# Optimization experiments

Measured on AMD Instinct MI355X. Metric: run time of the kernel, lower is better.

## Reference

```python
import jax, jax.numpy as jnp
import numpy as np

NUM_GROUPS = 32
NUM_HEADS = 8  # channels=512 / num_head_channels=64
EPS = 1e-5


def group_norm(x, gamma, beta):
    # x: [B, C, T]
    b, c, t = x.shape
    xg = x.reshape(b, NUM_GROUPS, (c // NUM_GROUPS) * t)
    mean = xg.mean(axis=-1, keepdims=True)
    var = xg.var(axis=-1, keepdims=True)
    xg = (xg - mean) * jax.lax.rsqrt(var + EPS)
    return xg.reshape(b, c, t) * gamma[None, :, None] + beta[None, :, None]


def setup_inputs() -> dict:
    key = jax.random.key(0)
    ks = jax.random.split(key, 8)
    B, C, H, W = 16, 512, 32, 32
    E = 1024
    x = jax.random.normal(ks[0], (B, C, H, W), dtype=jnp.float32)
    emb = jax.random.normal(ks[1], (B, E), dtype=jnp.float32)
    gn_gamma = jnp.ones((C,), jnp.float32)
    gn_beta = jnp.zeros((C,), jnp.float32)
    # FiLM: Linear(emb_channels, 2*channels), weight init std=0.001, bias zero
    emb_w = jax.random.normal(ks[2], (2 * C, E), dtype=jnp.float32) * 0.001
    emb_b = jnp.zeros((2 * C,), jnp.float32)
    # conv1x1 qkv: [3C, C]
    qkv_w = jax.random.normal(ks[3], (3 * C, C), dtype=jnp.float32) * (1.0 / np.sqrt(C))
    qkv_b = jnp.zeros((3 * C,), jnp.float32)
    # proj_out conv1x1 (zero-init in original; use small random so grads flow)
    proj_w = jax.random.normal(ks[4], (C, C), dtype=jnp.float32) * 0.02
    proj_b = jnp.zeros((C,), jnp.float32)
    return dict(x=x, emb=emb, gn_gamma=gn_gamma, gn_beta=gn_beta,
                emb_w=emb_w, emb_b=emb_b, qkv_w=qkv_w, qkv_b=qkv_b,
                proj_w=proj_w, proj_b=proj_b)


def reference(x, emb, gn_gamma, gn_beta, emb_w, emb_b, qkv_w, qkv_b, proj_w, proj_b):
    b, c, h_sp, w_sp = x.shape
    t = h_sp * w_sp
    xr = x.reshape(b, c, t)
    h = group_norm(xr, gn_gamma, gn_beta)
    # FiLM conditioning
    e = jax.nn.silu(emb) @ emb_w.T + emb_b  # [B, 2C]
    scale, shift = jnp.split(e, 2, axis=1)
    h = h * (1.0 + scale[:, :, None]) + shift[:, :, None]
    # conv1x1 QKV
    qkv = jnp.einsum('oc,bct->bot', qkv_w, h) + qkv_b[None, :, None]  # [B, 3C, T]
    ch = c // NUM_HEADS
    qkv = qkv.reshape(b * NUM_HEADS, 3 * ch, t)  # legacy head ordering
    q, k, v = jnp.split(qkv, 3, axis=1)
    s = 1.0 / jnp.sqrt(jnp.sqrt(jnp.float32(ch)))
    w = jnp.einsum('bct,bcs->bts', q * s, k * s)  # [B*H, T, T]
    w = jax.nn.softmax(w, axis=-1)
    a = jnp.einsum('bts,bcs->bct', w, v).reshape(b, c, t)
    out = jnp.einsum('oc,bct->bot', proj_w, a) + proj_b[None, :, None]
    return (xr + out).reshape(b, c, h_sp, w_sp)
```

## Files before the change

kernel.cpp:

```cpp
#include <hip/hip_runtime.h>
#include <hip/hip_bf16.h>

typedef __hip_bfloat16 bf16;
typedef __attribute__((ext_vector_type(8))) short short8;
typedef __attribute__((ext_vector_type(4))) float f32x4;
typedef __attribute__((ext_vector_type(4))) unsigned short us4;
typedef __attribute__((ext_vector_type(2))) unsigned short us2;

#define B_  16
#define C_  512
#define T_  1024
#define G_  32
#define CPG 16
#define E_  1024
#define NH  8
#define CH  64
#define CT  (C_ * T_)

__device__ __forceinline__ float b2f(bf16 v) { return __bfloat162float(v); }
__device__ __forceinline__ unsigned short fbits_fast(float v) {
  unsigned int u = __builtin_bit_cast(unsigned int, v);
  u += 0x7fff + ((u >> 16) & 1);
  return (unsigned short)(u >> 16);
}
__device__ __forceinline__ bf16 f2b_fast(float v) {
  unsigned short s = fbits_fast(v);
  return *reinterpret_cast<bf16*>(&s);
}
__device__ __forceinline__ unsigned int cvtpk(float lo, float hi) {
  unsigned int r;
  asm("v_cvt_pk_bf16_f32 %0, %1, %2" : "=v"(r) : "v"(lo), "v"(hi));
  return r;
}

__device__ __forceinline__ void gload16(const void* g, void* l) {
  __builtin_amdgcn_global_load_lds(
      (const __attribute__((address_space(1))) void*)g,
      (__attribute__((address_space(3))) void*)l, 16, 0, 0);
}

__global__ __launch_bounds__(256) void convert_w_kernel(
    const float* __restrict__ qkv_w, const float* __restrict__ proj_w,
    bf16* __restrict__ wq, bf16* __restrict__ wp) {
  int i4 = blockIdx.x * 256 + threadIdx.x;
  const int NQ4 = (3 * C_ * C_) / 4;
  const float* src;
  unsigned short* dst;
  int off;
  if (i4 < NQ4) {
    src = qkv_w; dst = (unsigned short*)wq; off = i4;
  } else {
    src = proj_w; dst = (unsigned short*)wp; off = i4 - NQ4;
  }
  float4 v = *(const float4*)(src + (size_t)off * 4);
  uint2 pk = {cvtpk(v.x, v.y), cvtpk(v.z, v.w)};
  *(uint2*)(dst + (size_t)off * 4) = pk;
}

__global__ __launch_bounds__(256) void convert_one(
    const float* __restrict__ src, bf16* __restrict__ dst) {
  int i4 = blockIdx.x * 256 + threadIdx.x;
  float4 v = *(const float4*)(src + (size_t)i4 * 4);
  uint2 pk = {cvtpk(v.x, v.y), cvtpk(v.z, v.w)};
  *(uint2*)((unsigned short*)dst + (size_t)i4 * 4) = pk;
}

__global__ __launch_bounds__(256) void film2_kernel(
    const float* __restrict__ emb, const float* __restrict__ emb_w,
    const float* __restrict__ emb_b, float* __restrict__ e_out) {
  __shared__ float S[B_ * E_];
  int tid = threadIdx.x;
  float4* S4 = (float4*)S;
  const float4* e4 = (const float4*)emb;
  for (int i = tid; i < (B_ * E_) / 4; i += 256) {
    float4 v = e4[i];
    float4 o;
    o.x = v.x / (1.f + __expf(-v.x));
    o.y = v.y / (1.f + __expf(-v.y));
    o.z = v.z / (1.f + __expf(-v.z));
    o.w = v.w / (1.f + __expf(-v.w));
    S4[i] = o;
  }
  __syncthreads();
  int wave = tid >> 6, lane = tid & 63;
  int j = blockIdx.x * 4 + wave;
  const float4* w4p = (const float4*)(emb_w + (size_t)j * E_);
  float4 w4[4];
#pragma unroll
  for (int k = 0; k < 4; k++) w4[k] = w4p[k * 64 + lane];
  float bias = emb_b[j];
  for (int b = 0; b < B_; b++) {
    const float4* Sb = (const float4*)(S + b * E_);
    float acc = 0.f;
#pragma unroll
    for (int k = 0; k < 4; k++) {
      float4 s = Sb[k * 64 + lane];
      acc += w4[k].x * s.x + w4[k].y * s.y + w4[k].z * s.z + w4[k].w * s.w;
    }
#pragma unroll
    for (int off = 1; off < 64; off <<= 1) acc += __shfl_xor(acc, off, 64);
    if (lane == 0) e_out[b * (2 * C_) + j] = acc + bias;
  }
}

__global__ __launch_bounds__(1024) void gn_stats_kernel(
    const float* __restrict__ x, float* __restrict__ mean_buf,
    float* __restrict__ rstd_buf) {
  int bg = blockIdx.x;
  const float4* b4 = (const float4*)(x + (size_t)bg * (CPG * T_));
  int tid = threadIdx.x;
  float s = 0.f, sq = 0.f;
#pragma unroll
  for (int p = 0; p < 4; p++) {
    float4 v = b4[p * 1024 + tid];
    s += v.x + v.y + v.z + v.w;
    sq += v.x * v.x + v.y * v.y + v.z * v.z + v.w * v.w;
  }
  for (int off = 32; off > 0; off >>= 1) {
    s += __shfl_down(s, off, 64);
    sq += __shfl_down(sq, off, 64);
  }
  __shared__ float ss[16], ssq[16];
  int wid = tid >> 6, lane = tid & 63;
  if (lane == 0) { ss[wid] = s; ssq[wid] = sq; }
  __syncthreads();
  if (tid == 0) {
    float S = 0.f, Q = 0.f;
#pragma unroll
    for (int w = 0; w < 16; w++) { S += ss[w]; Q += ssq[w]; }
    const float inv_n = 1.f / (CPG * T_);
    float m = S * inv_n;
    float var = Q * inv_n - m * m;
    mean_buf[bg] = m;
    rstd_buf[bg] = rsqrtf(fmaxf(var, 0.f) + 1e-5f);
  }
}

__global__ __launch_bounds__(256) void norm_film_t2(
    const float* __restrict__ x, const float* __restrict__ mean_buf,
    const float* __restrict__ rstd_buf, const float* __restrict__ gamma,
    const float* __restrict__ beta, const float* __restrict__ e_buf,
    bf16* __restrict__ h, int b0) {
  __shared__ unsigned short S[64][66];
  __shared__ float pm[64], pr[64], pa[64];
  int t0 = blockIdx.x * 64;
  int c0 = blockIdx.y * 64;
  int bl = blockIdx.z;
  int b = b0 + bl;
  int tid = threadIdx.x;
  if (tid < 64) {
    int c = c0 + tid;
    int g = c >> 4;
    float m = mean_buf[b * G_ + g];
    float r = rstd_buf[b * G_ + g];
    float sc = 1.f + e_buf[b * 2 * C_ + c];
    float sh = e_buf[b * 2 * C_ + C_ + c];
    pm[tid] = m;
    pr[tid] = r * gamma[c] * sc;
    pa[tid] = beta[c] * sc + sh;
  }
  __syncthreads();
  const float* xb = x + ((size_t)b * C_ + c0) * T_ + t0;
#pragma unroll
  for (int p = 0; p < 4; p++) {
    int i = p * 256 + tid;
    int cl = i >> 4, t4 = (i & 15) * 4;
    float4 v = *(const float4*)(xb + (size_t)cl * T_ + t4);
    float m = pm[cl], r = pr[cl], ad = pa[cl];
    *(unsigned int*)&S[cl][t4] = cvtpk((v.x - m) * r + ad, (v.y - m) * r + ad);
    *(unsigned int*)&S[cl][t4 + 2] =
        cvtpk((v.z - m) * r + ad, (v.w - m) * r + ad);
  }
  __syncthreads();
  unsigned short* hg = (unsigned short*)h + ((size_t)bl * T_ + t0) * C_ + c0;
#pragma unroll
  for (int p = 0; p < 2; p++) {
    int i = p * 256 + tid;
    int tr = i >> 3, c8 = (i & 7) * 8;
    unsigned int w0 = (unsigned int)S[c8 + 0][tr] |
                      ((unsigned int)S[c8 + 1][tr] << 16);
    unsigned int w1 = (unsigned int)S[c8 + 2][tr] |
                      ((unsigned int)S[c8 + 3][tr] << 16);
    unsigned int w2 = (unsigned int)S[c8 + 4][tr] |
                      ((unsigned int)S[c8 + 5][tr] << 16);
    unsigned int w3 = (unsigned int)S[c8 + 6][tr] |
                      ((unsigned int)S[c8 + 7][tr] << 16);
    int4 pk = {(int)w0, (int)w1, (int)w2, (int)w3};
    *(int4*)(hg + (size_t)tr * C_ + c8) = pk;
  }
}

#define ST_STRIDE 264
__global__ __launch_bounds__(256) void qkv_gemm_mfma5(
    const bf16* __restrict__ h, const bf16* __restrict__ wq,
    const float* __restrict__ qkv_b, bf16* __restrict__ qb,
    bf16* __restrict__ kb, bf16* __restrict__ vb, int ngroups) {
  __shared__ __align__(16) unsigned short LB[40960];
  int bid = blockIdx.x;
  int g, o;
  if ((ngroups & 7) == 0) {
    int xcd = bid & 7, j = bid >> 3;
    o = j % 24;
    int slot = j / 24;
    g = slot * 8 + xcd;
  } else {
    o = bid % 24;
    g = bid / 24;
  }
  int tst = g & 3;
  int bl = g >> 2;
  int o0 = o * 64;
  int tb = tst * 256;
  int tid = threadIdx.x;
  int wave = tid >> 6, lane = tid & 63;
  int col = lane & 15, quad = lane >> 4;
  int cs = col & 7;
  int w64 = wave * 64;
  const unsigned short* hg = (const unsigned short*)h + (size_t)bl * T_ * C_;
  const unsigned short* wg = (const unsigned short*)wq;
  char* lds = (char*)LB;
  f32x4 acc[4][4];
  for (int i = 0; i < 4; i++)
    for (int j2 = 0; j2 < 4; j2++) acc[i][j2] = f32x4{0, 0, 0, 0};

#define QSTAGE(buf, c0_)                                                      \
  do {                                                                        \
    _Pragma("unroll") for (int p = 0; p < 8; p++) {                           \
      int i_ = p * 256 + tid;                                                 \
      int row_ = i_ >> 3;                                                     \
      int sci_ = (i_ & 7) ^ (row_ & 7);                                       \
      gload16(hg + (size_t)(tb + row_) * C_ + (c0_) + sci_ * 8,               \
              lds + (buf) * 40960 + (p * 256 + wave * 64) * 16);              \
    }                                                                         \
    _Pragma("unroll") for (int p = 0; p < 2; p++) {                           \
      int i_ = p * 256 + tid;                                                 \
      int row_ = i_ >> 3;                                                     \
      int sci_ = (i_ & 7) ^ (row_ & 7);                                       \
      gload16(wg + (size_t)(o0 + row_) * C_ + (c0_) + sci_ * 8,               \
              lds + (buf) * 40960 + 32768 + (p * 256 + wave * 64) * 16);      \
    }                                                                         \
  } while (0)

  QSTAGE(0, 0);
  __syncthreads();
  int cur = 0;
  for (int kst = 0; kst < 8; kst++) {
    if (kst < 7) QSTAGE(cur ^ 1, (kst + 1) * 64);
    const unsigned short* hb = LB + cur * 20480;
    const unsigned short* wb2 = hb + 16384;
    __builtin_amdgcn_s_setprio(1);
#pragma unroll
    for (int ks = 0; ks < 2; ks++) {
      short8 af[4], bfr[4];
#pragma unroll
      for (int mt = 0; mt < 4; mt++)
        af[mt] = *(const short8*)&hb[(w64 + mt * 16 + col) * 64 +
                                     (((ks * 4 + quad) ^ cs) << 3)];
#pragma unroll
      for (int nt = 0; nt < 4; nt++)
        bfr[nt] = *(const short8*)&wb2[(nt * 16 + col) * 64 +
                                       (((ks * 4 + quad) ^ cs) << 3)];
#pragma unroll
      for (int mt = 0; mt < 4; mt++)
#pragma unroll
        for (int nt = 0; nt < 4; nt++)
          acc[mt][nt] = __builtin_amdgcn_mfma_f32_16x16x32_bf16(
              af[mt], bfr[nt], acc[mt][nt], 0, 0, 0);
    }
    __builtin_amdgcn_s_setprio(0);
    __syncthreads();
    cur ^= 1;
  }
#undef QSTAGE
  int sec = (o0 >> 6) % 3;
  int hd = o0 / 192;
  const float s = 0.35355339059327373f;
  const float sq = s * 1.4426950408889634f;
  if (sec < 2) {
    bf16* dst = (sec == 0) ? qb : kb;
    float sc = (sec == 0) ? sq : s;
    size_t hb2 = (size_t)(bl * NH + hd) * T_ * CH;
    for (int mt = 0; mt < 4; mt++) {
      for (int r = 0; r < 4; r++) {
        int t = tb + w64 + mt * 16 + quad * 4 + r;
        for (int nt = 0; nt < 4; nt++) {
          int ch = nt * 16 + col;
          dst[hb2 + (size_t)t * CH + ch] =
              f2b_fast((acc[mt][nt][r] + qkv_b[o0 + ch]) * sc);
        }
      }
    }
  } else {
    for (int mt = 0; mt < 4; mt++) {
      for (int r = 0; r < 4; r++) {
        int tl = w64 + mt * 16 + quad * 4 + r;
        for (int nt = 0; nt < 4; nt++) {
          int ch = nt * 16 + col;
          LB[ch * ST_STRIDE + tl] =
              fbits_fast(acc[mt][nt][r] + qkv_b[o0 + ch]);
        }
      }
    }
    __syncthreads();
    int rr = tid >> 2, csx = (tid & 3) * 64;
    size_t base = ((size_t)(bl * NH + hd) * CH + rr) * T_ + tb + csx;
    unsigned short* vg = (unsigned short*)vb;
    for (int j2 = 0; j2 < 8; j2++)
      *(int4*)(vg + base + j2 * 8) =
          *(const int4*)&LB[rr * ST_STRIDE + csx + j2 * 8];
  }
}

__global__ __launch_bounds__(256, 4) void attn_mfma8(
    const bf16* __restrict__ qb, const bf16* __restrict__ kb,
    const bf16* __restrict__ vb, bf16* __restrict__ a, int nbh) {
  __shared__ __align__(16) unsigned short LB[20480];
  int bid = blockIdx.x;
  int bh = bid % nbh;
  int qt0 = (bid / nbh) * 128;
  int tid = threadIdx.x;
  int wave = tid >> 6, lane = tid & 63;
  int col = lane & 15, quad = lane >> 4;
  int cs = col & 7;
  int ps = (col >> 1) & 3;
  const unsigned short* qg = (const unsigned short*)qb;
  const unsigned short* kg = (const unsigned short*)kb;
  const unsigned short* vg = (const unsigned short*)vb;
  const size_t tmaj = (size_t)bh * T_ * CH;
  const size_t cmaj = (size_t)bh * CH * T_;
  char* lds = (char*)LB;

  int qrow = qt0 + wave * 16 + col;
  short8 bq0[2], bq1[2];
#pragma unroll
  for (int u = 0; u < 2; u++) {
    const unsigned short* qp = qg + tmaj + (size_t)(qrow + u * 64) * CH;
    bq0[u] = *(const short8*)(qp + quad * 8);
    bq1[u] = *(const short8*)(qp + 32 + quad * 8);
  }
  f32x4 Ot0[4], Ot1[4];
#pragma unroll
  for (int mt = 0; mt < 4; mt++) {
    Ot0[mt] = f32x4{0, 0, 0, 0};
    Ot1[mt] = f32x4{0, 0, 0, 0};
  }
  const short ob = (short)0x3F80;
  short8 ones = {ob, ob, ob, ob, ob, ob, ob, ob};
  f32x4 La0 = f32x4{0, 0, 0, 0}, La1 = f32x4{0, 0, 0, 0};
  unsigned short* pw0 = LB + 16384 + wave * 512 + col * 32;
  unsigned short* pw1 = pw0 + 2048;

#define STAGE(buf, tt)                                                        \
  do {                                                                        \
    int s0_ = (tt) * 64;                                                      \
    const unsigned short* kt_ = kg + tmaj + (size_t)s0_ * CH;                 \
    const unsigned short* vt_ = vg + cmaj + s0_;                              \
    _Pragma("unroll") for (int cc = 0; cc < 2; cc++) {                        \
      int i_ = cc * 256 + tid;                                                \
      int row_ = i_ >> 3;                                                     \
      int sci_ = (i_ & 7) ^ (row_ & 7);                                       \
      int wb_ = (cc * 256 + wave * 64) * 16;       \
      gload16(kt_ + (size_t)row_ * CH + sci_ * 8, lds + (buf) * 8192 + wb_);  \
      gload16(vt_ + (size_t)row_ * T_ + sci_ * 8,                             \
              lds + 16384 + (buf) * 8192 + wb_);                              \
    }                                                                         \
  } while (0)

  STAGE(0, 0);
  __syncthreads();
  int cur = 0;
  for (int t = 0; t < 16; t++) {
    if (t < 15) STAGE(cur ^ 1, t + 1);
    const char* ksb = lds + cur * 8192;
    const char* vtb = lds + 16384 + cur * 8192;
    f32x4 St0[4], St1[4];
#pragma unroll
    for (int mt = 0; mt < 4; mt++) {
      St0[mt] = f32x4{0, 0, 0, 0};
      St1[mt] = f32x4{0, 0, 0, 0};
    }
    __builtin_amdgcn_s_setprio(1);
#pragma unroll
    for (int mt = 0; mt < 4; mt++) {
      int rb = (mt * 16 + col) * 128;
      short8 ak0 = *(const short8*)(ksb + rb + ((quad ^ cs) << 4));
      short8 ak1 = *(const short8*)(ksb + rb + (((quad + 4) ^ cs) << 4));
      St0[mt] = __builtin_amdgcn_mfma_f32_16x16x32_bf16(ak0, bq0[0], St0[mt], 0, 0, 0);
      St1[mt] = __builtin_amdgcn_mfma_f32_16x16x32_bf16(ak0, bq0[1], St1[mt], 0, 0, 0);
      St0[mt] = __builtin_amdgcn_mfma_f32_16x16x32_bf16(ak1, bq1[0], St0[mt], 0, 0, 0);
      St1[mt] = __builtin_amdgcn_mfma_f32_16x16x32_bf16(ak1, bq1[1], St1[mt], 0, 0, 0);
    }
    __builtin_amdgcn_s_setprio(0);
#pragma unroll
    for (int mt = 0; mt < 4; mt++)
#pragma unroll
      for (int r = 0; r < 4; r++) {
        St0[mt][r] = __builtin_amdgcn_exp2f(St0[mt][r]);
        St1[mt][r] = __builtin_amdgcn_exp2f(St1[mt][r]);
      }
#pragma unroll
    for (int kc = 0; kc < 2; kc++) {
#pragma unroll
      for (int mh = 0; mh < 2; mh++) {
        int mt = kc * 2 + mh;
        int wsw = (((2 * mh + (quad >> 1)) ^ ps) << 3) + (quad & 1) * 4;
        uint2 k0 = {cvtpk(St0[mt][0], St0[mt][1]),
                    cvtpk(St0[mt][2], St0[mt][3])};
        uint2 k1 = {cvtpk(St1[mt][0], St1[mt][1]),
                    cvtpk(St1[mt][2], St1[mt][3])};
        *(uint2*)(pw0 + wsw) = k0;
        *(uint2*)(pw1 + wsw) = k1;
      }
      int rsw = (quad ^ ps) << 3;
      short8 bp0 = *(const short8*)(pw0 + rsw);
      short8 bp1 = *(const short8*)(pw1 + rsw);
      __builtin_amdgcn_s_setprio(1);
      La0 = __builtin_amdgcn_mfma_f32_16x16x32_bf16(ones, bp0, La0, 0, 0, 0);
      La1 = __builtin_amdgcn_mfma_f32_16x16x32_bf16(ones, bp1, La1, 0, 0, 0);
#pragma unroll
      for (int mt = 0; mt < 4; mt++) {
        short8 av = *(const short8*)(vtb + (mt * 16 + col) * 128 +
                                     (((kc * 4 + quad) ^ cs) << 4));
        Ot0[mt] = __builtin_amdgcn_mfma_f32_16x16x32_bf16(av, bp0, Ot0[mt], 0, 0, 0);
        Ot1[mt] = __builtin_amdgcn_mfma_f32_16x16x32_bf16(av, bp1, Ot1[mt], 0, 0, 0);
      }
      __builtin_amdgcn_s_setprio(0);
    }
    __syncthreads();
    cur ^= 1;
  }
#undef STAGE
  int bl = bh >> 3, hd = bh & 7;
  unsigned short* ag = (unsigned short*)a;
#pragma unroll
  for (int u = 0; u < 2; u++) {
    float inv = 1.f / ((u == 0) ? La0[0] : La1[0]);
    const f32x4* Ou = (u == 0) ? Ot0 : Ot1;
    size_t rowb = ((size_t)bl * T_ + qrow + u * 64) * C_ + hd * CH;
#pragma unroll
    for (int mt = 0; mt < 4; mt++) {
      uint2 pk = {cvtpk(Ou[mt][0] * inv, Ou[mt][1] * inv),
                  cvtpk(Ou[mt][2] * inv, Ou[mt][3] * inv)};
      *(uint2*)(ag + rowb + mt * 16 + quad * 4) = pk;
    }
  }
}

__global__ __launch_bounds__(256) void proj_mfma4(
    const bf16* __restrict__ a, const bf16* __restrict__ wp,
    const float* __restrict__ proj_b, const float* __restrict__ x,
    float* __restrict__ out, int b0) {
  __shared__ __align__(16) unsigned short LB[16384];
  int bl = blockIdx.z;
  int b = b0 + bl;
  int o0 = blockIdx.y * 64;
  int t0 = blockIdx.x * 64;
  int tid = threadIdx.x;
  int wave = tid >> 6, lane = tid & 63;
  int col = lane & 15, quad = lane >> 4;
  int cs = col & 7;
  int m0 = wave * 16;
  const unsigned short* ag = (const unsigned short*)a + (size_t)bl * T_ * C_;
  const unsigned short* wg = (const unsigned short*)wp;
  char* lds = (char*)LB;
  f32x4 acc[4] = {f32x4{0,0,0,0}, f32x4{0,0,0,0}, f32x4{0,0,0,0}, f32x4{0,0,0,0}};

#define PSTAGE(buf, c0_)                                                      \
  do {                                                                        \
    _Pragma("unroll") for (int cc = 0; cc < 2; cc++) {                        \
      int i_ = cc * 256 + tid;                                                \
      int row_ = i_ >> 3;                                                     \
      int sci_ = (i_ & 7) ^ (row_ & 7);                                       \
      int wb_ = (cc * 256 + wave * 64) * 16;                                  \
      gload16(ag + (size_t)(t0 + row_) * C_ + (c0_) + sci_ * 8,               \
              lds + (buf) * 16384 + wb_);                                     \
      gload16(wg + (size_t)(o0 + row_) * C_ + (c0_) + sci_ * 8,               \
              lds + (buf) * 16384 + 8192 + wb_);                              \
    }                                                                         \
  } while (0)

  PSTAGE(0, 0);
  __syncthreads();
  int cur = 0;
  for (int kst = 0; kst < 8; kst++) {
    if (kst < 7) PSTAGE(cur ^ 1, (kst + 1) * 64);
    const unsigned short* ab = LB + cur * 8192;
    const unsigned short* wb2 = ab + 4096;
    __builtin_amdgcn_s_setprio(1);
#pragma unroll
    for (int ks = 0; ks < 2; ks++) {
      short8 aw = *(const short8*)&wb2[(m0 + col) * 64 +
                                       (((ks * 4 + quad) ^ cs) << 3)];
#pragma unroll
      for (int nt = 0; nt < 4; nt++) {
        short8 ba = *(const short8*)&ab[(nt * 16 + col) * 64 +
                                        (((ks * 4 + quad) ^ cs) << 3)];
        acc[nt] = __builtin_amdgcn_mfma_f32_16x16x32_bf16(aw, ba, acc[nt], 0, 0, 0);
      }
    }
    __builtin_amdgcn_s_setprio(0);
    __syncthreads();
    cur ^= 1;
  }
#undef PSTAGE
  for (int r = 0; r < 4; r++) {
    int o = o0 + m0 + quad * 4 + r;
    float bias = proj_b[o];
    size_t rowb = ((size_t)b * C_ + o) * T_ + t0;
    for (int nt = 0; nt < 4; nt++) {
      int t = nt * 16 + col;
      out[rowb + t] = x[rowb + t] + acc[nt][r] + bias;
    }
  }
}

extern "C" void kernel_launch(void* const* d_in, const int* in_sizes, int n_in,
                              void* d_out, int out_size, void* d_ws,
                              size_t ws_size, hipStream_t stream) {
  const float* x      = (const float*)d_in[0];
  const float* emb    = (const float*)d_in[1];
  const float* gamma  = (const float*)d_in[2];
  const float* beta   = (const float*)d_in[3];
  const float* emb_w  = (const float*)d_in[4];
  const float* emb_b  = (const float*)d_in[5];
  const float* qkv_w  = (const float*)d_in[6];
  const float* qkv_b  = (const float*)d_in[7];
  const float* proj_w = (const float*)d_in[8];
  const float* proj_b = (const float*)d_in[9];
  float* out = (float*)d_out;

  const size_t BUF16 = (size_t)16 * CT * sizeof(bf16);
  const size_t FULL4 = 4 * BUF16;
  const size_t SCR   = 131072 + (size_t)4 * C_ * C_ * sizeof(bf16);

  if (ws_size >= FULL4) {
    bf16* h_buf = (bf16*)d_ws;
    bf16* q_buf = h_buf + BUF16 / sizeof(bf16);
    bf16* k_buf = q_buf + BUF16 / sizeof(bf16);
    bf16* v_buf = k_buf + BUF16 / sizeof(bf16);
    bool inWs = ws_size >= FULL4 + SCR;
    char* scr = inWs ? ((char*)d_ws + FULL4) : (char*)d_out;
    float* e_buf    = (float*)scr;
    float* mean_buf = e_buf + B_ * 2 * C_;
    float* rstd_buf = mean_buf + B_ * G_;
    bf16*  wq_bf    = (bf16*)(scr + 131072);
    bf16*  wp_bf;

    if (inWs) {
      wp_bf = wq_bf + (size_t)3 * C_ * C_;
      convert_w_kernel<<<dim3(1024), 256, 0, stream>>>(qkv_w, proj_w, wq_bf,
                                                       wp_bf);
    } else {
      wp_bf = q_buf;
      convert_one<<<dim3(768), 256, 0, stream>>>(qkv_w, wq_bf);
    }
    film2_kernel<<<dim3(256), 256, 0, stream>>>(emb, emb_w, emb_b, e_buf);
    gn_stats_kernel<<<dim3(B_ * G_), 1024, 0, stream>>>(x, mean_buf, rstd_buf);
    norm_film_t2<<<dim3(16, 8, 16), 256, 0, stream>>>(
        x, mean_buf, rstd_buf, gamma, beta, e_buf, h_buf, 0);
    qkv_gemm_mfma5<<<dim3(24 * 64), 256, 0, stream>>>(h_buf, wq_bf, qkv_b,
                                                      q_buf, k_buf, v_buf, 64);
    attn_mfma8<<<dim3(8 * 128), 256, 0, stream>>>(q_buf, k_buf, v_buf, h_buf,
                                                  128);
    if (!inWs)
      convert_one<<<dim3(256), 256, 0, stream>>>(proj_w, wp_bf);
    proj_mfma4<<<dim3(16, 8, 16), 256, 0, stream>>>(h_buf, wp_bf, proj_b, x,
                                                    out, 0);
  } else {
    float* e_buf    = (float*)d_ws;
    float* mean_buf = e_buf + B_ * 2 * C_;
    float* rstd_buf = mean_buf + B_ * G_;
    bf16*  wq_bf    = (bf16*)((char*)d_ws + 131072);
    bf16*  wp_bf    = wq_bf + (size_t)3 * C_ * C_;
    bf16* pool = (bf16*)((char*)d_ws + SCR);
    size_t avail = ws_size > SCR ? ws_size - SCR : 0;
    int NB = 16;
    while (NB > 1 && (size_t)4 * NB * CT * sizeof(bf16) > avail) NB >>= 1;
    bf16* h_buf = pool;
    bf16* q_buf = h_buf + (size_t)NB * CT;
    bf16* k_buf = q_buf + (size_t)NB * CT;
    bf16* v_buf = k_buf + (size_t)NB * CT;

    convert_w_kernel<<<dim3(1024), 256, 0, stream>>>(qkv_w, proj_w, wq_bf,
                                                     wp_bf);
    film2_kernel<<<dim3(256), 256, 0, stream>>>(emb, emb_w, emb_b, e_buf);
    gn_stats_kernel<<<dim3(B_ * G_), 1024, 0, stream>>>(x, mean_buf, rstd_buf);
    for (int b0 = 0; b0 < B_; b0 += NB) {
      norm_film_t2<<<dim3(16, 8, NB), 256, 0, stream>>>(
          x, mean_buf, rstd_buf, gamma, beta, e_buf, h_buf, b0);
      qkv_gemm_mfma5<<<dim3(24 * 4 * NB), 256, 0, stream>>>(
          h_buf, wq_bf, qkv_b, q_buf, k_buf, v_buf, 4 * NB);
      int nbh = NB * NH;
      attn_mfma8<<<dim3(8 * nbh), 256, 0, stream>>>(q_buf, k_buf, v_buf,
                                                    h_buf, nbh);
      proj_mfma4<<<dim3(16, 8, NB), 256, 0, stream>>>(h_buf, wp_bf, proj_b, x,
                                                      out, b0);
    }
  }
}
```

Baseline: 223.4 us.

## Fuse prep kernels and load attention V directly to registers

```diff
diff --git a/kernel.cpp b/kernel.cpp
--- a/kernel.cpp
+++ b/kernel.cpp
@@ -39,22 +39,96 @@
       (__attribute__((address_space(3))) void*)l, 16, 0, 0);
 }
 
-__global__ __launch_bounds__(256) void convert_w_kernel(
+__global__ __launch_bounds__(1024) void prep_kernel(
     const float* __restrict__ qkv_w, const float* __restrict__ proj_w,
-    bf16* __restrict__ wq, bf16* __restrict__ wp) {
-  int i4 = blockIdx.x * 256 + threadIdx.x;
-  const int NQ4 = (3 * C_ * C_) / 4;
-  const float* src;
-  unsigned short* dst;
-  int off;
-  if (i4 < NQ4) {
-    src = qkv_w; dst = (unsigned short*)wq; off = i4;
-  } else {
-    src = proj_w; dst = (unsigned short*)wp; off = i4 - NQ4;
-  }
-  float4 v = *(const float4*)(src + (size_t)off * 4);
-  uint2 pk = {cvtpk(v.x, v.y), cvtpk(v.z, v.w)};
-  *(uint2*)(dst + (size_t)off * 4) = pk;
+    bf16* __restrict__ wq, bf16* __restrict__ wp,
+    const float* __restrict__ emb, const float* __restrict__ emb_w,
+    const float* __restrict__ emb_b, float* __restrict__ e_out,
+    const float* __restrict__ x, float* __restrict__ mean_buf,
+    float* __restrict__ rstd_buf, int nconv) {
+  __shared__ float S[B_ * E_];
+  __shared__ float ss[16], ssq[16];
+  int bid = blockIdx.x;
+  int tid = threadIdx.x;
+  if (bid < nconv) {
+    int i4 = bid * 1024 + tid;
+    const int NQ4 = (3 * C_ * C_) / 4;
+    const float* src;
+    unsigned short* dst;
+    int off;
+    if (i4 < NQ4) {
+      src = qkv_w; dst = (unsigned short*)wq; off = i4;
+    } else {
+      src = proj_w; dst = (unsigned short*)wp; off = i4 - NQ4;
+    }
+    float4 v = *(const float4*)(src + (size_t)off * 4);
+    uint2 pk = {cvtpk(v.x, v.y), cvtpk(v.z, v.w)};
+    *(uint2*)(dst + (size_t)off * 4) = pk;
+    return;
+  }
+  bid -= nconv;
+  int wave = tid >> 6, lane = tid & 63;
+  if (bid < 64) {
+    float4* S4 = (float4*)S;
+    const float4* e4 = (const float4*)emb;
+    for (int i = tid; i < (B_ * E_) / 4; i += 1024) {
+      float4 v = e4[i];
+      float4 o;
+      o.x = v.x / (1.f + __expf(-v.x));
+      o.y = v.y / (1.f + __expf(-v.y));
+      o.z = v.z / (1.f + __expf(-v.z));
+      o.w = v.w / (1.f + __expf(-v.w));
+      S4[i] = o;
+    }
+    __syncthreads();
+    int j = bid * 16 + wave;
+    const float4* w4p = (const float4*)(emb_w + (size_t)j * E_);
+    float4 w4[4];
+#pragma unroll
+    for (int k = 0; k < 4; k++) w4[k] = w4p[k * 64 + lane];
+    float bias = emb_b[j];
+    for (int b = 0; b < B_; b++) {
+      const float4* Sb = (const float4*)(S + b * E_);
+      float acc = 0.f;
+#pragma unroll
+      for (int k = 0; k < 4; k++) {
+        float4 s = Sb[k * 64 + lane];
+        acc += w4[k].x * s.x + w4[k].y * s.y + w4[k].z * s.z + w4[k].w * s.w;
+      }
+#pragma unroll
+      for (int off = 1; off < 64; off <<= 1) acc += __shfl_xor(acc, off, 64);
+      if (lane == 0) e_out[b * (2 * C_) + j] = acc + bias;
+    }
+    return;
+  }
+  bid -= 64;
+  {
+    int bg = bid;
+    const float4* b4 = (const float4*)(x + (size_t)bg * (CPG * T_));
+    float s = 0.f, sq = 0.f;
+#pragma unroll
+    for (int p = 0; p < 4; p++) {
+      float4 v = b4[p * 1024 + tid];
+      s += v.x + v.y + v.z + v.w;
+      sq += v.x * v.x + v.y * v.y + v.z * v.z + v.w * v.w;
+    }
+    for (int off = 32; off > 0; off >>= 1) {
+      s += __shfl_down(s, off, 64);
+      sq += __shfl_down(sq, off, 64);
+    }
+    if (lane == 0) { ss[wave] = s; ssq[wave] = sq; }
+    __syncthreads();
+    if (tid == 0) {
+      float Sm = 0.f, Q = 0.f;
+#pragma unroll
+      for (int w = 0; w < 16; w++) { Sm += ss[w]; Q += ssq[w]; }
+      const float inv_n = 1.f / (CPG * T_);
+      float m = Sm * inv_n;
+      float var = Q * inv_n - m * m;
+      mean_buf[bg] = m;
+      rstd_buf[bg] = rsqrtf(fmaxf(var, 0.f) + 1e-5f);
+    }
+  }
 }
 
 __global__ __launch_bounds__(256) void convert_one(
@@ -63,77 +137,6 @@
   float4 v = *(const float4*)(src + (size_t)i4 * 4);
   uint2 pk = {cvtpk(v.x, v.y), cvtpk(v.z, v.w)};
   *(uint2*)((unsigned short*)dst + (size_t)i4 * 4) = pk;
-}
-
-__global__ __launch_bounds__(256) void film2_kernel(
-    const float* __restrict__ emb, const float* __restrict__ emb_w,
-    const float* __restrict__ emb_b, float* __restrict__ e_out) {
-  __shared__ float S[B_ * E_];
-  int tid = threadIdx.x;
-  float4* S4 = (float4*)S;
-  const float4* e4 = (const float4*)emb;
-  for (int i = tid; i < (B_ * E_) / 4; i += 256) {
-    float4 v = e4[i];
-    float4 o;
-    o.x = v.x / (1.f + __expf(-v.x));
-    o.y = v.y / (1.f + __expf(-v.y));
-    o.z = v.z / (1.f + __expf(-v.z));
-    o.w = v.w / (1.f + __expf(-v.w));
-    S4[i] = o;
-  }
-  __syncthreads();
-  int wave = tid >> 6, lane = tid & 63;
-  int j = blockIdx.x * 4 + wave;
-  const float4* w4p = (const float4*)(emb_w + (size_t)j * E_);
-  float4 w4[4];
-#pragma unroll
-  for (int k = 0; k < 4; k++) w4[k] = w4p[k * 64 + lane];
-  float bias = emb_b[j];
-  for (int b = 0; b < B_; b++) {
-    const float4* Sb = (const float4*)(S + b * E_);
-    float acc = 0.f;
-#pragma unroll
-    for (int k = 0; k < 4; k++) {
-      float4 s = Sb[k * 64 + lane];
-      acc += w4[k].x * s.x + w4[k].y * s.y + w4[k].z * s.z + w4[k].w * s.w;
-    }
-#pragma unroll
-    for (int off = 1; off < 64; off <<= 1) acc += __shfl_xor(acc, off, 64);
-    if (lane == 0) e_out[b * (2 * C_) + j] = acc + bias;
-  }
-}
-
-__global__ __launch_bounds__(1024) void gn_stats_kernel(
-    const float* __restrict__ x, float* __restrict__ mean_buf,
-    float* __restrict__ rstd_buf) {
-  int bg = blockIdx.x;
-  const float4* b4 = (const float4*)(x + (size_t)bg * (CPG * T_));
-  int tid = threadIdx.x;
-  float s = 0.f, sq = 0.f;
-#pragma unroll
-  for (int p = 0; p < 4; p++) {
-    float4 v = b4[p * 1024 + tid];
-    s += v.x + v.y + v.z + v.w;
-    sq += v.x * v.x + v.y * v.y + v.z * v.z + v.w * v.w;
-  }
-  for (int off = 32; off > 0; off >>= 1) {
-    s += __shfl_down(s, off, 64);
-    sq += __shfl_down(sq, off, 64);
-  }
-  __shared__ float ss[16], ssq[16];
-  int wid = tid >> 6, lane = tid & 63;
-  if (lane == 0) { ss[wid] = s; ssq[wid] = sq; }
-  __syncthreads();
-  if (tid == 0) {
-    float S = 0.f, Q = 0.f;
-#pragma unroll
-    for (int w = 0; w < 16; w++) { S += ss[w]; Q += ssq[w]; }
-    const float inv_n = 1.f / (CPG * T_);
-    float m = S * inv_n;
-    float var = Q * inv_n - m * m;
-    mean_buf[bg] = m;
-    rstd_buf[bg] = rsqrtf(fmaxf(var, 0.f) + 1e-5f);
-  }
 }
 
 __global__ __launch_bounds__(256) void norm_film_t2(
@@ -311,10 +314,10 @@
   }
 }
 
-__global__ __launch_bounds__(256, 4) void attn_mfma8(
+__global__ __launch_bounds__(256, 4) void attn_mfma9(
     const bf16* __restrict__ qb, const bf16* __restrict__ kb,
     const bf16* __restrict__ vb, bf16* __restrict__ a, int nbh) {
-  __shared__ __align__(16) unsigned short LB[20480];
+  __shared__ __align__(16) unsigned short LB[12288];
   int bid = blockIdx.x;
   int bh = bid % nbh;
   int qt0 = (bid / nbh) * 128;
@@ -347,46 +350,46 @@
   const short ob = (short)0x3F80;
   short8 ones = {ob, ob, ob, ob, ob, ob, ob, ob};
   f32x4 La0 = f32x4{0, 0, 0, 0}, La1 = f32x4{0, 0, 0, 0};
-  unsigned short* pw0 = LB + 16384 + wave * 512 + col * 32;
+  const f32x4 z4 = {0.f, 0.f, 0.f, 0.f};
+  unsigned short* pw0 = LB + 8192 + wave * 512 + col * 32;
   unsigned short* pw1 = pw0 + 2048;
 
-#define STAGE(buf, tt)                                                        \
+#define KSTAGE(buf, tt)                                                       \
   do {                                                                        \
     int s0_ = (tt) * 64;                                                      \
     const unsigned short* kt_ = kg + tmaj + (size_t)s0_ * CH;                 \
-    const unsigned short* vt_ = vg + cmaj + s0_;                              \
     _Pragma("unroll") for (int cc = 0; cc < 2; cc++) {                        \
       int i_ = cc * 256 + tid;                                                \
       int row_ = i_ >> 3;                                                     \
       int sci_ = (i_ & 7) ^ (row_ & 7);                                       \
-      int wb_ = (cc * 256 + wave * 64) * 16;       \
-      gload16(kt_ + (size_t)row_ * CH + sci_ * 8, lds + (buf) * 8192 + wb_);  \
-      gload16(vt_ + (size_t)row_ * T_ + sci_ * 8,                             \
-              lds + 16384 + (buf) * 8192 + wb_);                              \
+      gload16(kt_ + (size_t)row_ * CH + sci_ * 8,                             \
+              lds + (buf) * 8192 + (cc * 256 + wave * 64) * 16);              \
     }                                                                         \
   } while (0)
 
-  STAGE(0, 0);
+  KSTAGE(0, 0);
   __syncthreads();
   int cur = 0;
   for (int t = 0; t < 16; t++) {
-    if (t < 15) STAGE(cur ^ 1, t + 1);
+    int s0 = t * 64;
+    short8 avv[8];
+#pragma unroll
+    for (int kc = 0; kc < 2; kc++)
+#pragma unroll
+      for (int mt = 0; mt < 4; mt++)
+        avv[kc * 4 + mt] = *(const short8*)(
+            vg + cmaj + (size_t)(mt * 16 + col) * T_ + s0 + kc * 32 + quad * 8);
+    if (t < 15) KSTAGE(cur ^ 1, t + 1);
     const char* ksb = lds + cur * 8192;
-    const char* vtb = lds + 16384 + cur * 8192;
     f32x4 St0[4], St1[4];
-#pragma unroll
-    for (int mt = 0; mt < 4; mt++) {
-      St0[mt] = f32x4{0, 0, 0, 0};
-      St1[mt] = f32x4{0, 0, 0, 0};
-    }
     __builtin_amdgcn_s_setprio(1);
 #pragma unroll
     for (int mt = 0; mt < 4; mt++) {
       int rb = (mt * 16 + col) * 128;
       short8 ak0 = *(const short8*)(ksb + rb + ((quad ^ cs) << 4));
       short8 ak1 = *(const short8*)(ksb + rb + (((quad + 4) ^ cs) << 4));
-      St0[mt] = __builtin_amdgcn_mfma_f32_16x16x32_bf16(ak0, bq0[0], St0[mt], 0, 0, 0);
-      St1[mt] = __builtin_amdgcn_mfma_f32_16x16x32_bf16(ak0, bq0[1], St1[mt], 0, 0, 0);
+      St0[mt] = __builtin_amdgcn_mfma_f32_16x16x32_bf16(ak0, bq0[0], z4, 0, 0, 0);
+      St1[mt] = __builtin_amdgcn_mfma_f32_16x16x32_bf16(ak0, bq0[1], z4, 0, 0, 0);
       St0[mt] = __builtin_amdgcn_mfma_f32_16x16x32_bf16(ak1, bq1[0], St0[mt], 0, 0, 0);
       St1[mt] = __builtin_amdgcn_mfma_f32_16x16x32_bf16(ak1, bq1[1], St1[mt], 0, 0, 0);
     }
@@ -419,17 +422,17 @@
       La1 = __builtin_amdgcn_mfma_f32_16x16x32_bf16(ones, bp1, La1, 0, 0, 0);
 #pragma unroll
       for (int mt = 0; mt < 4; mt++) {
-        short8 av = *(const short8*)(vtb + (mt * 16 + col) * 128 +
-                                     (((kc * 4 + quad) ^ cs) << 4));
-        Ot0[mt] = __builtin_amdgcn_mfma_f32_16x16x32_bf16(av, bp0, Ot0[mt], 0, 0, 0);
-        Ot1[mt] = __builtin_amdgcn_mfma_f32_16x16x32_bf16(av, bp1, Ot1[mt], 0, 0, 0);
+        Ot0[mt] = __builtin_amdgcn_mfma_f32_16x16x32_bf16(avv[kc * 4 + mt],
+                                                          bp0, Ot0[mt], 0, 0, 0);
+        Ot1[mt] = __builtin_amdgcn_mfma_f32_16x16x32_bf16(avv[kc * 4 + mt],
+                                                          bp1, Ot1[mt], 0, 0, 0);
       }
       __builtin_amdgcn_s_setprio(0);
     }
     __syncthreads();
     cur ^= 1;
   }
-#undef STAGE
+#undef KSTAGE
   int bl = bh >> 3, hd = bh & 7;
   unsigned short* ag = (unsigned short*)a;
 #pragma unroll
@@ -545,22 +548,22 @@
     float* rstd_buf = mean_buf + B_ * G_;
     bf16*  wq_bf    = (bf16*)(scr + 131072);
     bf16*  wp_bf;
-
+    int nconv;
     if (inWs) {
       wp_bf = wq_bf + (size_t)3 * C_ * C_;
-      convert_w_kernel<<<dim3(1024), 256, 0, stream>>>(qkv_w, proj_w, wq_bf,
-                                                       wp_bf);
+      nconv = 256;
     } else {
       wp_bf = q_buf;
-      convert_one<<<dim3(768), 256, 0, stream>>>(qkv_w, wq_bf);
-    }
-    film2_kernel<<<dim3(256), 256, 0, stream>>>(emb, emb_w, emb_b, e_buf);
-    gn_stats_kernel<<<dim3(B_ * G_), 1024, 0, stream>>>(x, mean_buf, rstd_buf);
+      nconv = 192;
+    }
+    prep_kernel<<<dim3(nconv + 64 + 512), 1024, 0, stream>>>(
+        qkv_w, proj_w, wq_bf, wp_bf, emb, emb_w, emb_b, e_buf, x, mean_buf,
+        rstd_buf, nconv);
     norm_film_t2<<<dim3(16, 8, 16), 256, 0, stream>>>(
         x, mean_buf, rstd_buf, gamma, beta, e_buf, h_buf, 0);
     qkv_gemm_mfma5<<<dim3(24 * 64), 256, 0, stream>>>(h_buf, wq_bf, qkv_b,
                                                       q_buf, k_buf, v_buf, 64);
-    attn_mfma8<<<dim3(8 * 128), 256, 0, stream>>>(q_buf, k_buf, v_buf, h_buf,
+    attn_mfma9<<<dim3(8 * 128), 256, 0, stream>>>(q_buf, k_buf, v_buf, h_buf,
                                                   128);
     if (!inWs)
       convert_one<<<dim3(256), 256, 0, stream>>>(proj_w, wp_bf);
@@ -581,17 +584,16 @@
     bf16* k_buf = q_buf + (size_t)NB * CT;
     bf16* v_buf = k_buf + (size_t)NB * CT;
 
-    convert_w_kernel<<<dim3(1024), 256, 0, stream>>>(qkv_w, proj_w, wq_bf,
-                                                     wp_bf);
-    film2_kernel<<<dim3(256), 256, 0, stream>>>(emb, emb_w, emb_b, e_buf);
-    gn_stats_kernel<<<dim3(B_ * G_), 1024, 0, stream>>>(x, mean_buf, rstd_buf);
+    prep_kernel<<<dim3(256 + 64 + 512), 1024, 0, stream>>>(
+        qkv_w, proj_w, wq_bf, wp_bf, emb, emb_w, emb_b, e_buf, x, mean_buf,
+        rstd_buf, 256);
     for (int b0 = 0; b0 < B_; b0 += NB) {
       norm_film_t2<<<dim3(16, 8, NB), 256, 0, stream>>>(
           x, mean_buf, rstd_buf, gamma, beta, e_buf, h_buf, b0);
       qkv_gemm_mfma5<<<dim3(24 * 4 * NB), 256, 0, stream>>>(
           h_buf, wq_bf, qkv_b, q_buf, k_buf, v_buf, 4 * NB);
       int nbh = NB * NH;
-      attn_mfma8<<<dim3(8 * nbh), 256, 0, stream>>>(q_buf, k_buf, v_buf,
+      attn_mfma9<<<dim3(8 * nbh), 256, 0, stream>>>(q_buf, k_buf, v_buf,
                                                     h_buf, nbh);
       proj_mfma4<<<dim3(16, 8, NB), 256, 0, stream>>>(h_buf, wp_bf, proj_b, x,
                                                       out, b0);
```

New measurement: 305.6 us. 36.8% more time.
